# Kernel optimization log

Hardware: AMD Instinct MI355X
Metric: run time of the kernel (lower is better)

The kernel has to match this reference:

```python
import jax, jax.numpy as jnp
import numpy as np

N, E, F_NODE, F_EDGE, H = 50000, 800000, 64, 32, 64
NT, ET, ETE = 3, 4, 4  # num node types, num edge types, edge-type embedding dim
NEG = 0.2              # leaky_relu negative slope (PyG HEATConv default)


def hetero_lin(x, t, W, b):
    # per-type linear: x [N,in], t [N] int, W [T,in,out], b [T,out]
    outs = jnp.einsum('ni,tio->tno', x, W) + b[:, None, :]   # [T,N,out]
    return outs[t, jnp.arange(x.shape[0])]                   # [N,out]


def segment_softmax(logits, seg, num_segments):
    m = jax.ops.segment_max(logits, seg, num_segments=num_segments)
    ex = jnp.exp(logits - m[seg])
    s = jax.ops.segment_sum(ex, seg, num_segments=num_segments)
    return ex / (s[seg] + 1e-16)


def eheat_conv(x, src, dst, node_type, edge_type, edge_attr, Whl, bhl, Ete, Wea, Watt, Wlin):
    n = x.shape[0]
    h = hetero_lin(x, node_type, Whl, bhl)            # [N,H]
    ete = jax.nn.leaky_relu(Ete[edge_type], NEG)      # [E,ETE]
    ea = jax.nn.leaky_relu(edge_attr @ Wea, NEG)      # [E,H] edge embedding (returned)
    xi, xj = h[dst], h[src]                           # gather target/source node feats
    # attention logits = leaky_relu(att(cat([x_i, x_j, ete, ea]))); Watt split to avoid big concat
    Wi, Wj, Wt, We = Watt[:H], Watt[H:2 * H], Watt[2 * H:2 * H + ETE], Watt[2 * H + ETE:]
    logits = jax.nn.leaky_relu(xi @ Wi + xj @ Wj + ete @ Wt + ea @ We, NEG)[:, 0]  # [E]
    alpha = segment_softmax(logits, dst, n)           # softmax over incoming edges of dst
    # message = lin(cat([x_j, ea])) * alpha ; scatter-add at dst (heads=1, dropout eval=identity)
    msg = (xj @ Wlin[:H] + ea @ Wlin[H:]) * alpha[:, None]   # [E,H]
    out = jax.ops.segment_sum(msg, dst, num_segments=n)     # [N,H]
    return out, ea


def setup_inputs():
    key = jax.random.key(0)
    ks = jax.random.split(key, 40)
    def rnd(i, shape):
        return jax.random.normal(ks[i], shape, dtype=jnp.float32) * 0.1
    inp = {
        'x': jax.random.normal(ks[0], (N, F_NODE), dtype=jnp.float32),
        'edge_index': jax.random.randint(ks[1], (2, E), 0, N),
        'node_type': jax.random.randint(ks[2], (N,), 0, NT),
        'edge_type': jax.random.randint(ks[3], (E,), 0, ET),
        'edge_attr': jax.random.normal(ks[4], (E, F_EDGE), dtype=jnp.float32),
    }
    node_ins = [F_NODE, H, H]
    edge_ins = [F_EDGE, H, H]
    i = 5
    for l in range(3):
        inp[f'Whl{l+1}'] = rnd(i, (NT, node_ins[l], H)); i += 1
        inp[f'bhl{l+1}'] = jnp.zeros((NT, H), jnp.float32)
        inp[f'Ete{l+1}'] = rnd(i, (ET, ETE)); i += 1
        inp[f'Wea{l+1}'] = rnd(i, (edge_ins[l], H)); i += 1
        inp[f'Watt{l+1}'] = rnd(i, (2 * H + ETE + H, 1)); i += 1
        inp[f'Wlin{l+1}'] = rnd(i, (2 * H, H)); i += 1
    inp['Wnc'] = rnd(i, (NT, H, 1)); i += 1
    inp['bnc'] = jnp.zeros((NT, 1), jnp.float32)
    inp['Wec'] = rnd(i, (ET, H, 1)); i += 1
    inp['bec'] = jnp.zeros((ET, 1), jnp.float32)
    return inp


def reference(x, edge_index, node_type, edge_type, edge_attr,
              Whl1, bhl1, Ete1, Wea1, Watt1, Wlin1,
              Whl2, bhl2, Ete2, Wea2, Watt2, Wlin2,
              Whl3, bhl3, Ete3, Wea3, Watt3, Wlin3,
              Wnc, bnc, Wec, bec):
    src, dst = edge_index[0], edge_index[1]
    h, e = eheat_conv(x, src, dst, node_type, edge_type, edge_attr,
                      Whl1, bhl1, Ete1, Wea1, Watt1, Wlin1)
    h, e = jax.nn.relu(h), jax.nn.relu(e)   # dropout is identity in eval mode
    h, e = eheat_conv(h, src, dst, node_type, edge_type, e,
                      Whl2, bhl2, Ete2, Wea2, Watt2, Wlin2)
    h, e = jax.nn.relu(h), jax.nn.relu(e)
    h, e = eheat_conv(h, src, dst, node_type, edge_type, e,
                      Whl3, bhl3, Ete3, Wea3, Watt3, Wlin3)
    h, e = jax.nn.relu(h), jax.nn.relu(e)
    x_out = hetero_lin(h, node_type, Wnc, bnc)   # [N,1]
    e_out = hetero_lin(e, edge_type, Wec, bec)   # [E,1]
    return (x_out, e_out)
```

## Files before the change

### kernel.cpp

```cpp
#include <hip/hip_runtime.h>
#include <hip/hip_bf16.h>

#define NEG 0.2f
#define LRELU(x) ((x) > 0.f ? (x) : NEG*(x))

typedef __hip_bfloat16 bf16;
typedef __attribute__((ext_vector_type(8))) short short8v;
typedef __attribute__((ext_vector_type(4))) float f32x4;

__device__ __forceinline__ float b2f(bf16 v){ return __bfloat162float(v); }
__device__ __forceinline__ float ldf(const float* p, size_t i){ return p[i]; }
__device__ __forceinline__ float ldf(const bf16* p, size_t i){ return __bfloat162float(p[i]); }

__device__ __forceinline__ float wred(float v){
#pragma unroll
  for(int o=32;o>0;o>>=1) v += __shfl_down(v,o);
  return v;
}

__device__ __forceinline__ int atomAddI(int* p, int v){
  return __hip_atomic_fetch_add(p, v, __ATOMIC_RELAXED, __HIP_MEMORY_SCOPE_AGENT);
}


__global__ __launch_bounds__(256) void k_hist(
    const int* __restrict__ dst, int* __restrict__ deg, int nE)
{
  int e = blockIdx.x*blockDim.x + threadIdx.x;
  if (e >= nE) return;
  atomAddI(&deg[dst[e]], 1);
}

__global__ __launch_bounds__(1024) void k_scan(
    const int* __restrict__ deg, int* __restrict__ off, int nN)
{
  __shared__ int part[1024];
  int tid = threadIdx.x;
  int chunk = (nN + 1023) / 1024;
  int lo = tid*chunk, hi = min((tid+1)*chunk, nN);
  int s = 0;
  for (int i=lo;i<hi;i++) s += deg[i];
  part[tid] = s;
  __syncthreads();
  for (int d=1; d<1024; d<<=1){
    int v = (tid>=d) ? part[tid-d] : 0;
    __syncthreads();
    part[tid] += v;
    __syncthreads();
  }
  int run = (tid==0) ? 0 : part[tid-1];
  for (int i=lo;i<hi;i++){ off[i] = run; run += deg[i]; }
  if (tid==1023) off[nN] = part[1023];
}

__global__ __launch_bounds__(256) void k_scatter(
    const int* __restrict__ dst, const int* __restrict__ off,
    int* __restrict__ cnt, int* __restrict__ eid, int nE)
{
  int e = blockIdx.x*blockDim.x + threadIdx.x;
  if (e >= nE) return;
  int d = dst[e];
  int p = atomAddI(&cnt[d], 1);
  eid[off[d] + p] = e;
}

__global__ __launch_bounds__(256) void k_perm(
    const int* __restrict__ eid, const int* __restrict__ src,
    const int* __restrict__ dst, const int* __restrict__ ety,
    int* __restrict__ srcP, int* __restrict__ dstP, int* __restrict__ etyP, int nE)
{
  int i = blockIdx.x*blockDim.x + threadIdx.x;
  if (i >= nE) return;
  int e = eid[i];
  srcP[i] = src[e];
  dstP[i] = dst[e];
  etyP[i] = ety[e];
}


template<typename TIN, bool RELU_IN>
__global__ __launch_bounds__(256) void k_hlin(
    const TIN* __restrict__ xin, const int* __restrict__ ntype,
    const float* __restrict__ Whl, const float* __restrict__ bhl,
    const float* __restrict__ Watt,
    bf16* __restrict__ h, float* __restrict__ hi_s, float* __restrict__ hj_s,
    int nN)
{
  int wid  = (blockIdx.x*blockDim.x + threadIdx.x) >> 6;
  int lane = threadIdx.x & 63;
  if (wid >= nN) return;
  int t = ntype[wid];
  float xv = ldf(xin, (size_t)wid*64 + lane);
  if (RELU_IN) xv = fmaxf(xv, 0.f);
  const float* W = Whl + (size_t)t*4096;
  float acc = bhl[t*64 + lane];
#pragma unroll
  for (int i=0;i<64;i++) acc = fmaf(__shfl(xv, i), W[i*64 + lane], acc);
  h[(size_t)wid*64 + lane] = __float2bfloat16(acc);
  float pi = wred(acc * Watt[lane]);
  float pj = wred(acc * Watt[64 + lane]);
  if (lane==0){ hi_s[wid]=pi; hj_s[wid]=pj; }
}

__global__ __launch_bounds__(256) void k_bfrag(
    const float* __restrict__ W, bf16* __restrict__ frag, int KS)
{
  int t = blockIdx.x*blockDim.x + threadIdx.x;
  int total = 4*KS*64;
  if (t >= total) return;
  int lane = t & 63;
  int ks = (t>>6) % KS;
  int nt = (t>>6) / KS;
  int kb = lane>>4, col = lane&15;
#pragma unroll
  for (int j=0;j<8;j++){
    frag[((size_t)(nt*KS+ks)*64 + lane)*8 + j] =
      __float2bfloat16(W[(ks*32 + kb*8 + j)*64 + nt*16 + col]);
  }
}

template<int LAYER>
__global__ __launch_bounds__(256) void k_ea_mfma(
    const void* __restrict__ ain_, const int* __restrict__ eid,
    const bf16* __restrict__ bfrag, const float* __restrict__ Watt,
    const int* __restrict__ srcP, const int* __restrict__ dstP,
    const int* __restrict__ etyP, const float* __restrict__ Ete,
    const float* __restrict__ hi_s, const float* __restrict__ hj_s,
    bf16* __restrict__ eaS, float* __restrict__ exS,
    const float* __restrict__ Wec, const float* __restrict__ bec,
    float* __restrict__ e_out, int nE)
{
  constexpr int KS = (LAYER==0) ? 1 : 2;
  int wid  = (blockIdx.x*blockDim.x + threadIdx.x) >> 6;
  int lane = threadIdx.x & 63;
  int e0 = wid * 32;
  if (e0 >= nE) return;
  int row = lane & 15;
  int kb  = lane >> 4;

  short8v a[2][KS];
#pragma unroll
  for (int tl=0; tl<2; tl++){
    int er = min(e0 + tl*16 + row, nE-1);
    if (LAYER==0) {
      const float* A = (const float*)ain_;
      const float* p = A + (size_t)eid[er]*32 + kb*8;
#pragma unroll
      for (int j=0;j<8;j++){
        bf16 b = __float2bfloat16(p[j]);
        a[tl][0][j] = *reinterpret_cast<short*>(&b);
      }
    } else {
      const bf16* A = (const bf16*)ain_;
#pragma unroll
      for (int ks=0; ks<KS; ks++){
        short8v v = *reinterpret_cast<const short8v*>(
            reinterpret_cast<const short*>(A + (size_t)er*64 + ks*32 + kb*8));
#pragma unroll
        for (int j=0;j<8;j++) v[j] = (v[j] & (short)0x8000) ? (short)0 : v[j];
        a[tl][ks] = v;
      }
    }
  }

  f32x4 acc[2][4];
#pragma unroll
  for (int nt=0; nt<4; nt++){
    f32x4 c0 = {0.f,0.f,0.f,0.f}, c1 = {0.f,0.f,0.f,0.f};
#pragma unroll
    for (int ks=0; ks<KS; ks++){
      short8v b = *reinterpret_cast<const short8v*>(
          reinterpret_cast<const short*>(bfrag) + (((size_t)nt*KS + ks)*64 + lane)*8);
      c0 = __builtin_amdgcn_mfma_f32_16x16x32_bf16(a[0][ks], b, c0, 0, 0, 0);
      c1 = __builtin_amdgcn_mfma_f32_16x16x32_bf16(a[1][ks], b, c1, 0, 0, 0);
    }
#pragma unroll
    for (int r=0;r<4;r++){ c0[r] = LRELU(c0[r]); c1[r] = LRELU(c1[r]); }
    acc[0][nt] = c0; acc[1][nt] = c1;
  }

#pragma unroll
  for (int tl=0; tl<2; tl++){
#pragma unroll
    for (int r=0;r<4;r++){
      int e = e0 + tl*16 + kb*4 + r;
      if (e < nE){
#pragma unroll
        for (int nt=0;nt<4;nt++)
          eaS[(size_t)e*64 + nt*16 + row] = __float2bfloat16(acc[tl][nt][r]);
      }
    }
  }

#pragma unroll
  for (int tl=0; tl<2; tl++){
#pragma unroll
    for (int r=0;r<4;r++){
      int e = e0 + tl*16 + kb*4 + r;
      bool valid = (e < nE);
      int t = valid ? etyP[e] : 0;
      float lp = 0.f, pe = 0.f;
#pragma unroll
      for (int nt=0;nt<4;nt++) lp = fmaf(acc[tl][nt][r], Watt[132 + nt*16 + row], lp);
      if (LAYER==2){
#pragma unroll
        for (int nt=0;nt<4;nt++) pe = fmaf(fmaxf(acc[tl][nt][r],0.f), Wec[t*64 + nt*16 + row], pe);
      }
#pragma unroll
      for (int m=1;m<16;m<<=1){
        lp += __shfl_xor(lp, m);
        if (LAYER==2) pe += __shfl_xor(pe, m);
      }
      if (row == 0 && valid){
        int d = dstP[e], s = srcP[e];
        float wt = 0.f;
#pragma unroll
        for (int k=0;k<4;k++){ float v = Ete[t*4+k]; v = LRELU(v); wt = fmaf(v, Watt[128+k], wt); }
        float l = lp + hi_s[d] + hj_s[s] + wt;
        l = LRELU(l);
        exS[e] = __expf(fminf(l, 60.f));
        if (LAYER==2) e_out[eid[e]] = pe + bec[t];
      }
    }
  }
}

__global__ __launch_bounds__(256) void k_agg(
    const int* __restrict__ off, const int* __restrict__ srcP,
    const bf16* __restrict__ h, const bf16* __restrict__ eaS,
    const float* __restrict__ exS,
    bf16* __restrict__ uv, int nN)
{
  int wid  = (blockIdx.x*blockDim.x + threadIdx.x) >> 6;
  int lane = threadIdx.x & 63;
  if (wid >= nN) return;
  int beg = off[wid], end = off[wid+1];
  float au = 0.f, av = 0.f, ss = 0.f;
  int i = beg;
  for (; i+1 < end; i += 2){
    int   s0 = srcP[i],   s1 = srcP[i+1];
    float a0 = exS[i],    a1 = exS[i+1];
    float h0 = b2f(h[(size_t)s0*64 + lane]);
    float h1 = b2f(h[(size_t)s1*64 + lane]);
    float v0 = b2f(eaS[(size_t)i*64 + lane]);
    float v1 = b2f(eaS[(size_t)(i+1)*64 + lane]);
    au = fmaf(a0, h0, au); av = fmaf(a0, v0, av); ss += a0;
    au = fmaf(a1, h1, au); av = fmaf(a1, v1, av); ss += a1;
  }
  if (i < end){
    int s = srcP[i]; float a = exS[i];
    au = fmaf(a, b2f(h[(size_t)s*64 + lane]), au);
    av = fmaf(a, b2f(eaS[(size_t)i*64 + lane]), av);
    ss += a;
  }
  float inv = 1.f / (ss + 1e-16f);
  uv[(size_t)wid*128 + lane]      = __float2bfloat16(au * inv);
  uv[(size_t)wid*128 + 64 + lane] = __float2bfloat16(av * inv);
}

template<bool FINAL>
__global__ __launch_bounds__(256) void k_mm_mfma(
    const bf16* __restrict__ uv, const bf16* __restrict__ bfrag,
    float* __restrict__ out,
    const int* __restrict__ ntype, const float* __restrict__ Wnc,
    const float* __restrict__ bnc, float* __restrict__ xout, int nN)
{
  int wid  = (blockIdx.x*blockDim.x + threadIdx.x) >> 6;
  int lane = threadIdx.x & 63;
  int n0 = wid * 16;
  if (n0 >= nN) return;
  int row = lane & 15;
  int kb  = lane >> 4;
  int nr  = min(n0 + row, nN-1);

  short8v a[4];
#pragma unroll
  for (int ks=0; ks<4; ks++)
    a[ks] = *reinterpret_cast<const short8v*>(
        reinterpret_cast<const short*>(uv + (size_t)nr*128 + ks*32 + kb*8));

  f32x4 acc[4];
#pragma unroll
  for (int nt=0; nt<4; nt++){
    f32x4 c = {0.f,0.f,0.f,0.f};
#pragma unroll
    for (int ks=0; ks<4; ks++){
      short8v b = *reinterpret_cast<const short8v*>(
          reinterpret_cast<const short*>(bfrag) + (((size_t)nt*4 + ks)*64 + lane)*8);
      c = __builtin_amdgcn_mfma_f32_16x16x32_bf16(a[ks], b, c, 0, 0, 0);
    }
    acc[nt] = c;
  }

  if (!FINAL){
#pragma unroll
    for (int r=0;r<4;r++){
      int n = n0 + kb*4 + r;
      if (n < nN){
#pragma unroll
        for (int nt=0;nt<4;nt++)
          out[(size_t)n*64 + nt*16 + row] = acc[nt][r];
      }
    }
  } else {
#pragma unroll
    for (int r=0;r<4;r++){
      int n = n0 + kb*4 + r;
      bool valid = (n < nN);
      int t = valid ? ntype[n] : 0;
      float pe = 0.f;
#pragma unroll
      for (int nt=0;nt<4;nt++)
        pe = fmaf(fmaxf(acc[nt][r],0.f), Wnc[t*64 + nt*16 + row], pe);
#pragma unroll
      for (int m=1;m<16;m<<=1) pe += __shfl_xor(pe, m);
      if (row == 0 && valid) xout[n] = pe + bnc[t];
    }
  }
}

extern "C" void kernel_launch(void* const* d_in, const int* in_sizes, int n_in,
                              void* d_out, int out_size, void* d_ws, size_t ws_size,
                              hipStream_t stream) {
  const float* x      = (const float*)d_in[0];
  const int*   eidx   = (const int*) d_in[1];
  const int*   ntype  = (const int*) d_in[2];
  const int*   etype  = (const int*) d_in[3];
  const float* eattr  = (const float*)d_in[4];
  const float* Whl[3]  = {(const float*)d_in[5],  (const float*)d_in[11], (const float*)d_in[17]};
  const float* bhl[3]  = {(const float*)d_in[6],  (const float*)d_in[12], (const float*)d_in[18]};
  const float* Ete[3]  = {(const float*)d_in[7],  (const float*)d_in[13], (const float*)d_in[19]};
  const float* Wea[3]  = {(const float*)d_in[8],  (const float*)d_in[14], (const float*)d_in[20]};
  const float* Watt[3] = {(const float*)d_in[9],  (const float*)d_in[15], (const float*)d_in[21]};
  const float* Wlin[3] = {(const float*)d_in[10], (const float*)d_in[16], (const float*)d_in[22]};
  const float* Wnc = (const float*)d_in[23];
  const float* bnc = (const float*)d_in[24];
  const float* Wec = (const float*)d_in[25];
  const float* bec = (const float*)d_in[26];

  const int nN = in_sizes[2];
  const int nE = in_sizes[3];
  const int* srcI = eidx;
  const int* dstI = eidx + nE;

  float* ws = (float*)d_ws;
  size_t o = 0;
  bf16*  h      = (bf16*)(ws + o); o += (size_t)nN*32;
  float* outA   = ws + o;
  bf16*  uv     = (bf16*)(ws + o); o += (size_t)nN*64;
  float* hi_s   = ws + o;          o += (size_t)nN;
  float* hj_s   = ws + o;          o += (size_t)nN;
  float* exS    = ws + o;          o += (size_t)nE;
  bf16*  eaS    = (bf16*)(ws + o); o += (size_t)nE*32;
  int*   deg    = (int*)(ws + o);  o += (size_t)nN;
  int*   off    = (int*)(ws + o);  o += (size_t)nN + 1;
  int*   eid    = (int*)(ws + o);  o += (size_t)nE;
  int*   srcP   = (int*)(ws + o);  o += (size_t)nE;
  int*   dstP   = (int*)(ws + o);  o += (size_t)nE;
  int*   etyP   = (int*)(ws + o);  o += (size_t)nE;
  o = (o + 3) & ~(size_t)3;
  bf16*  bfrag  = (bf16*)(ws + o); o += (size_t)4096;

  dim3 blk(256);
  int nodeWB = (int)(((size_t)nN*64 + 255)/256);
  int edgeTB = (nE + 255)/256;
  int eaMB   = (int)(((size_t)((nE+31)/32)*64 + 255)/256);
  int mmMB   = (int)(((size_t)((nN+15)/16)*64 + 255)/256);

  hipMemsetAsync(deg, 0, (size_t)nN*4, stream);
  k_hist<<<edgeTB, blk, 0, stream>>>(dstI, deg, nE);
  k_scan<<<1, 1024, 0, stream>>>(deg, off, nN);
  hipMemsetAsync(deg, 0, (size_t)nN*4, stream);
  k_scatter<<<edgeTB, blk, 0, stream>>>(dstI, off, deg, eid, nE);
  k_perm<<<edgeTB, blk, 0, stream>>>(eid, srcI, dstI, etype, srcP, dstP, etyP, nE);

  float* xout = (float*)d_out;

  for (int L = 0; L < 3; ++L) {
    if (L == 0)
      k_hlin<float,false><<<nodeWB, blk, 0, stream>>>(x,    ntype, Whl[L], bhl[L], Watt[L], h, hi_s, hj_s, nN);
    else
      k_hlin<float,true ><<<nodeWB, blk, 0, stream>>>(outA, ntype, Whl[L], bhl[L], Watt[L], h, hi_s, hj_s, nN);

    int KS = (L==0) ? 1 : 2;
    k_bfrag<<<(4*KS*64 + 255)/256, blk, 0, stream>>>(Wea[L], bfrag, KS);
    if (L == 0)
      k_ea_mfma<0><<<eaMB, blk, 0, stream>>>(eattr, eid, bfrag, Watt[L], srcP, dstP, etyP, Ete[L],
                                             hi_s, hj_s, eaS, exS, nullptr, nullptr, nullptr, nE);
    else if (L == 1)
      k_ea_mfma<1><<<eaMB, blk, 0, stream>>>(eaS, eid, bfrag, Watt[L], srcP, dstP, etyP, Ete[L],
                                             hi_s, hj_s, eaS, exS, nullptr, nullptr, nullptr, nE);
    else
      k_ea_mfma<2><<<eaMB, blk, 0, stream>>>(eaS, eid, bfrag, Watt[L], srcP, dstP, etyP, Ete[L],
                                             hi_s, hj_s, eaS, exS, Wec, bec, xout + nN, nE);

    k_agg<<<nodeWB, blk, 0, stream>>>(off, srcP, h, eaS, exS, uv, nN);

    k_bfrag<<<(4*4*64 + 255)/256, blk, 0, stream>>>(Wlin[L], bfrag, 4);
    if (L < 2)
      k_mm_mfma<false><<<mmMB, blk, 0, stream>>>(uv, bfrag, outA, nullptr, nullptr, nullptr, nullptr, nN);
    else
      k_mm_mfma<true ><<<mmMB, blk, 0, stream>>>(uv, bfrag, nullptr, ntype, Wnc, bnc, xout, nN);
  }
}
```

Before: 913.1 us.

## Use MFMA for per-type node linear with nodes bucketed by type

Nodes are grouped by type into 32-padded buckets so the per-type hetero linear can run as bf16 MFMA tiles, with the attention projections folded into an extra output column tile. All weight fragments are precomputed once in a single prep kernel instead of per-layer k_bfrag launches. The attention logit combination is moved out of the edge MFMA kernel into a separate k_att kernel. This adds bucketing and prep kernels, one extra edge pass per layer, and bf16 rounding of the node inputs.

Measured after the change: 1.458 ms. 1.6x slower.

```diff
diff --git a/kernel.cpp b/kernel.cpp
--- a/kernel.cpp
+++ b/kernel.cpp
@@ -9,8 +9,6 @@
 typedef __attribute__((ext_vector_type(4))) float f32x4;
 
 __device__ __forceinline__ float b2f(bf16 v){ return __bfloat162float(v); }
-__device__ __forceinline__ float ldf(const float* p, size_t i){ return p[i]; }
-__device__ __forceinline__ float ldf(const bf16* p, size_t i){ return __bfloat162float(p[i]); }
 
 __device__ __forceinline__ float wred(float v){
 #pragma unroll
@@ -77,45 +75,146 @@
   etyP[i] = ety[e];
 }
 
-
-template<typename TIN, bool RELU_IN>
-__global__ __launch_bounds__(256) void k_hlin(
-    const TIN* __restrict__ xin, const int* __restrict__ ntype,
-    const float* __restrict__ Whl, const float* __restrict__ bhl,
-    const float* __restrict__ Watt,
-    bf16* __restrict__ h, float* __restrict__ hi_s, float* __restrict__ hj_s,
-    int nN)
+__global__ __launch_bounds__(256) void k_nhist(
+    const int* __restrict__ ntype, int* __restrict__ ndeg, int nN)
+{
+  int n = blockIdx.x*blockDim.x + threadIdx.x;
+  if (n >= nN) return;
+  atomAddI(&ndeg[ntype[n]], 1);
+}
+
+__global__ void k_npad(const int* __restrict__ ndeg, int* __restrict__ poffPad)
+{
+  if (threadIdx.x==0 && blockIdx.x==0){
+    int o = 0;
+#pragma unroll
+    for (int t=0;t<3;t++){ poffPad[t] = o; o += ((ndeg[t]+31)/32)*32; }
+    poffPad[3] = o;
+  }
+}
+
+__global__ __launch_bounds__(256) void k_nscatter(
+    const int* __restrict__ ntype, const int* __restrict__ poffPad,
+    int* __restrict__ ncnt, int* __restrict__ nPermPad, int nN)
+{
+  int n = blockIdx.x*blockDim.x + threadIdx.x;
+  if (n >= nN) return;
+  int t = ntype[n];
+  int p = atomAddI(&ncnt[t], 1);
+  nPermPad[poffPad[t] + p] = n;
+}
+
+struct BDesc { const float* W; const float* Wi; const float* Wj; int KS; int NT; int dstOff; };
+struct PrepArgs {
+  BDesc d[15];
+  const float* bhl[3];
+  const float* watt[3];
+};
+
+__global__ __launch_bounds__(256) void k_prep(
+    PrepArgs pa, bf16* __restrict__ fragBase, float* __restrict__ biasDot)
+{
+  int bid = blockIdx.x;
+  if (bid < 75){
+    int b = bid / 5;
+    int tid = (bid % 5)*256 + threadIdx.x;
+    BDesc d = pa.d[b];
+    int total = d.NT * d.KS * 64;
+    if (tid >= total) return;
+    int lane = tid & 63;
+    int ks = (tid>>6) % d.KS;
+    int nt = (tid>>6) / d.KS;
+    int kb = lane>>4, col16 = lane&15;
+    bf16* frag = fragBase + d.dstOff;
+#pragma unroll
+    for (int j=0;j<8;j++){
+      int k = ks*32 + kb*8 + j;
+      float val;
+      if (nt < 4) val = d.W[k*64 + nt*16 + col16];
+      else {
+        const float* v = (col16==0) ? d.Wi : (col16==1) ? d.Wj : nullptr;
+        val = 0.f;
+        if (v){ for (int c=0;c<64;c++) val = fmaf(d.W[k*64+c], v[c], val); }
+      }
+      frag[((size_t)(nt*d.KS+ks)*64 + lane)*8 + j] = __float2bfloat16(val);
+    }
+  } else {
+    int lane = threadIdx.x;
+    if (lane >= 64) return;
+    for (int idx=0; idx<18; idx++){
+      int L = idx/6, rem = idx%6, t = rem>>1, ij = rem&1;
+      float p = pa.bhl[L][t*64 + lane] * pa.watt[L][ij*64 + lane];
+      p = wred(p);
+      if (lane==0) biasDot[idx] = p;
+    }
+  }
+}
+
+
+template<bool RELU_IN>
+__global__ __launch_bounds__(256) void k_hlin_mfma(
+    const float* __restrict__ xin, const int* __restrict__ nPermPad,
+    const int* __restrict__ poffPad, const bf16* __restrict__ hlFragL,
+    const float* __restrict__ bhl, const float* __restrict__ biasDotL,
+    bf16* __restrict__ h, float* __restrict__ hi_s, float* __restrict__ hj_s)
 {
   int wid  = (blockIdx.x*blockDim.x + threadIdx.x) >> 6;
   int lane = threadIdx.x & 63;
-  if (wid >= nN) return;
-  int t = ntype[wid];
-  float xv = ldf(xin, (size_t)wid*64 + lane);
-  if (RELU_IN) xv = fmaxf(xv, 0.f);
-  const float* W = Whl + (size_t)t*4096;
-  float acc = bhl[t*64 + lane];
-#pragma unroll
-  for (int i=0;i<64;i++) acc = fmaf(__shfl(xv, i), W[i*64 + lane], acc);
-  h[(size_t)wid*64 + lane] = __float2bfloat16(acc);
-  float pi = wred(acc * Watt[lane]);
-  float pj = wred(acc * Watt[64 + lane]);
-  if (lane==0){ hi_s[wid]=pi; hj_s[wid]=pj; }
-}
-
-__global__ __launch_bounds__(256) void k_bfrag(
-    const float* __restrict__ W, bf16* __restrict__ frag, int KS)
-{
-  int t = blockIdx.x*blockDim.x + threadIdx.x;
-  int total = 4*KS*64;
-  if (t >= total) return;
-  int lane = t & 63;
-  int ks = (t>>6) % KS;
-  int nt = (t>>6) / KS;
-  int kb = lane>>4, col = lane&15;
-#pragma unroll
-  for (int j=0;j<8;j++){
-    frag[((size_t)(nt*KS+ks)*64 + lane)*8 + j] =
-      __float2bfloat16(W[(ks*32 + kb*8 + j)*64 + nt*16 + col]);
+  int n0 = wid * 32;
+  if (n0 >= poffPad[3]) return;
+  int t = (n0 >= poffPad[1]) + (n0 >= poffPad[2]);
+  const bf16* frag = hlFragL + (size_t)t*5120;
+  int row = lane & 15, kb = lane >> 4;
+
+  short8v a[2][2];
+#pragma unroll
+  for (int tl=0; tl<2; tl++){
+    int orig = nPermPad[n0 + tl*16 + row];
+    const float* p = xin + (size_t)max(orig,0)*64;
+#pragma unroll
+    for (int ks=0; ks<2; ks++){
+#pragma unroll
+      for (int j=0;j<8;j++){
+        float v = p[ks*32 + kb*8 + j];
+        if (RELU_IN) v = fmaxf(v, 0.f);
+        bf16 b = __float2bfloat16(v);
+        a[tl][ks][j] = *reinterpret_cast<short*>(&b);
+      }
+    }
+  }
+
+  f32x4 acc[2][5];
+#pragma unroll
+  for (int nt=0; nt<5; nt++){
+    f32x4 c0 = {0.f,0.f,0.f,0.f}, c1 = {0.f,0.f,0.f,0.f};
+#pragma unroll
+    for (int ks=0; ks<2; ks++){
+      short8v b = *reinterpret_cast<const short8v*>(
+          reinterpret_cast<const short*>(frag) + (((size_t)nt*2 + ks)*64 + lane)*8);
+      c0 = __builtin_amdgcn_mfma_f32_16x16x32_bf16(a[0][ks], b, c0, 0, 0, 0);
+      c1 = __builtin_amdgcn_mfma_f32_16x16x32_bf16(a[1][ks], b, c1, 0, 0, 0);
+    }
+    acc[0][nt] = c0; acc[1][nt] = c1;
+  }
+
+  float bb[4];
+#pragma unroll
+  for (int nt=0;nt<4;nt++) bb[nt] = bhl[t*64 + nt*16 + row];
+  float bdi = biasDotL[t*2+0], bdj = biasDotL[t*2+1];
+
+#pragma unroll
+  for (int tl=0; tl<2; tl++){
+#pragma unroll
+    for (int r=0;r<4;r++){
+      int orig = nPermPad[n0 + tl*16 + kb*4 + r];
+      if (orig >= 0){
+#pragma unroll
+        for (int nt=0;nt<4;nt++)
+          h[(size_t)orig*64 + nt*16 + row] = __float2bfloat16(acc[tl][nt][r] + bb[nt]);
+        if (row==0) hi_s[orig] = acc[tl][4][r] + bdi;
+        if (row==1) hj_s[orig] = acc[tl][4][r] + bdj;
+      }
+    }
   }
 }
 
@@ -123,10 +222,8 @@
 __global__ __launch_bounds__(256) void k_ea_mfma(
     const void* __restrict__ ain_, const int* __restrict__ eid,
     const bf16* __restrict__ bfrag, const float* __restrict__ Watt,
-    const int* __restrict__ srcP, const int* __restrict__ dstP,
-    const int* __restrict__ etyP, const float* __restrict__ Ete,
-    const float* __restrict__ hi_s, const float* __restrict__ hj_s,
-    bf16* __restrict__ eaS, float* __restrict__ exS,
+    const int* __restrict__ etyP,
+    bf16* __restrict__ eaS, float* __restrict__ lp,
     const float* __restrict__ Wec, const float* __restrict__ bec,
     float* __restrict__ e_out, int nE)
 {
@@ -198,31 +295,43 @@
     for (int r=0;r<4;r++){
       int e = e0 + tl*16 + kb*4 + r;
       bool valid = (e < nE);
-      int t = valid ? etyP[e] : 0;
-      float lp = 0.f, pe = 0.f;
-#pragma unroll
-      for (int nt=0;nt<4;nt++) lp = fmaf(acc[tl][nt][r], Watt[132 + nt*16 + row], lp);
-      if (LAYER==2){
-#pragma unroll
-        for (int nt=0;nt<4;nt++) pe = fmaf(fmaxf(acc[tl][nt][r],0.f), Wec[t*64 + nt*16 + row], pe);
+      float lpv = 0.f, pe = 0.f;
+      int t = 0;
+      if (LAYER==2) t = valid ? etyP[e] : 0;
+#pragma unroll
+      for (int nt=0;nt<4;nt++){
+        lpv = fmaf(acc[tl][nt][r], Watt[132 + nt*16 + row], lpv);
+        if (LAYER==2) pe = fmaf(fmaxf(acc[tl][nt][r],0.f), Wec[t*64 + nt*16 + row], pe);
       }
 #pragma unroll
       for (int m=1;m<16;m<<=1){
-        lp += __shfl_xor(lp, m);
+        lpv += __shfl_xor(lpv, m);
         if (LAYER==2) pe += __shfl_xor(pe, m);
       }
       if (row == 0 && valid){
-        int d = dstP[e], s = srcP[e];
-        float wt = 0.f;
-#pragma unroll
-        for (int k=0;k<4;k++){ float v = Ete[t*4+k]; v = LRELU(v); wt = fmaf(v, Watt[128+k], wt); }
-        float l = lp + hi_s[d] + hj_s[s] + wt;
-        l = LRELU(l);
-        exS[e] = __expf(fminf(l, 60.f));
+        lp[e] = lpv;
         if (LAYER==2) e_out[eid[e]] = pe + bec[t];
       }
     }
   }
+}
+
+__global__ __launch_bounds__(256) void k_att(
+    const int* __restrict__ srcP, const int* __restrict__ dstP,
+    const int* __restrict__ etyP, const float* __restrict__ Ete,
+    const float* __restrict__ Watt,
+    const float* __restrict__ hi_s, const float* __restrict__ hj_s,
+    float* __restrict__ lpex, int nE)
+{
+  int e = blockIdx.x*blockDim.x + threadIdx.x;
+  if (e >= nE) return;
+  int d = dstP[e], s = srcP[e], t = etyP[e];
+  float wt = 0.f;
+#pragma unroll
+  for (int k=0;k<4;k++){ float v = Ete[t*4+k]; v = LRELU(v); wt = fmaf(v, Watt[128+k], wt); }
+  float l = lpex[e] + hi_s[d] + hj_s[s] + wt;
+  l = LRELU(l);
+  lpex[e] = __expf(fminf(l, 60.f));
 }
 
 __global__ __launch_bounds__(256) void k_agg(
@@ -350,7 +459,7 @@
   bf16*  uv     = (bf16*)(ws + o); o += (size_t)nN*64;
   float* hi_s   = ws + o;          o += (size_t)nN;
   float* hj_s   = ws + o;          o += (size_t)nN;
-  float* exS    = ws + o;          o += (size_t)nE;
+  float* lpex   = ws + o;          o += (size_t)nE;
   bf16*  eaS    = (bf16*)(ws + o); o += (size_t)nE*32;
   int*   deg    = (int*)(ws + o);  o += (size_t)nN;
   int*   off    = (int*)(ws + o);  o += (size_t)nN + 1;
@@ -358,13 +467,24 @@
   int*   srcP   = (int*)(ws + o);  o += (size_t)nE;
   int*   dstP   = (int*)(ws + o);  o += (size_t)nE;
   int*   etyP   = (int*)(ws + o);  o += (size_t)nE;
+  int*   ndeg   = (int*)(ws + o);  o += 4;
+  int*   ncnt   = (int*)(ws + o);  o += 4;
+  int*   poffPad= (int*)(ws + o);  o += 4;
+  int*   nPermPad=(int*)(ws + o);  o += (size_t)nN + 96;
   o = (o + 3) & ~(size_t)3;
-  bf16*  bfrag  = (bf16*)(ws + o); o += (size_t)4096;
+  bf16*  fragB  = (bf16*)(ws + o); o += 40448;
+  float* biasDot= ws + o;          o += 18;
+
+  const int eaOff[3] = {0, 2048, 6144};
+  const int hlOff = 10240;
+  const int wlOff = 56320;
 
   dim3 blk(256);
   int nodeWB = (int)(((size_t)nN*64 + 255)/256);
   int edgeTB = (nE + 255)/256;
+  int nodeTB = (nN + 255)/256;
   int eaMB   = (int)(((size_t)((nE+31)/32)*64 + 255)/256);
+  int hlMB   = (int)(((size_t)((nN+96+31)/32)*64 + 255)/256);
   int mmMB   = (int)(((size_t)((nN+15)/16)*64 + 255)/256);
 
   hipMemsetAsync(deg, 0, (size_t)nN*4, stream);
@@ -374,32 +494,53 @@
   k_scatter<<<edgeTB, blk, 0, stream>>>(dstI, off, deg, eid, nE);
   k_perm<<<edgeTB, blk, 0, stream>>>(eid, srcI, dstI, etype, srcP, dstP, etyP, nE);
 
+  hipMemsetAsync(ndeg, 0, 8*4, stream);
+  k_nhist<<<nodeTB, blk, 0, stream>>>(ntype, ndeg, nN);
+  k_npad<<<1, 64, 0, stream>>>(ndeg, poffPad);
+  hipMemsetAsync(nPermPad, 0xFF, ((size_t)nN+96)*4, stream);
+  k_nscatter<<<nodeTB, blk, 0, stream>>>(ntype, poffPad, ncnt, nPermPad, nN);
+
+  PrepArgs pa;
+  pa.d[0] = {Wea[0], nullptr, nullptr, 1, 4, eaOff[0]};
+  pa.d[1] = {Wea[1], nullptr, nullptr, 2, 4, eaOff[1]};
+  pa.d[2] = {Wea[2], nullptr, nullptr, 2, 4, eaOff[2]};
+  for (int L=0; L<3; L++)
+    for (int t=0; t<3; t++)
+      pa.d[3 + L*3 + t] = {Whl[L] + (size_t)t*4096, Watt[L], Watt[L]+64, 2, 5, hlOff + (L*3+t)*5120};
+  for (int L=0; L<3; L++)
+    pa.d[12 + L] = {Wlin[L], nullptr, nullptr, 4, 4, wlOff + L*8192};
+  for (int L=0; L<3; L++){ pa.bhl[L] = bhl[L]; pa.watt[L] = Watt[L]; }
+  k_prep<<<76, blk, 0, stream>>>(pa, fragB, biasDot);
+
   float* xout = (float*)d_out;
 
   for (int L = 0; L < 3; ++L) {
     if (L == 0)
-      k_hlin<float,false><<<nodeWB, blk, 0, stream>>>(x,    ntype, Whl[L], bhl[L], Watt[L], h, hi_s, hj_s, nN);
+      k_hlin_mfma<false><<<hlMB, blk, 0, stream>>>(x,    nPermPad, poffPad, fragB + hlOff + L*3*5120,
+                                                   bhl[L], biasDot + L*6, h, hi_s, hj_s);
     else
-      k_hlin<float,true ><<<nodeWB, blk, 0, stream>>>(outA, ntype, Whl[L], bhl[L], Watt[L], h, hi_s, hj_s, nN);
-
-    int KS = (L==0) ? 1 : 2;
-    k_bfrag<<<(4*KS*64 + 255)/256, blk, 0, stream>>>(Wea[L], bfrag, KS);
+      k_hlin_mfma<true ><<<hlMB, blk, 0, stream>>>(outA, nPermPad, poffPad, fragB + hlOff + L*3*5120,
+                                                   bhl[L], biasDot + L*6, h, hi_s, hj_s);
+
     if (L == 0)
-      k_ea_mfma<0><<<eaMB, blk, 0, stream>>>(eattr, eid, bfrag, Watt[L], srcP, dstP, etyP, Ete[L],
-                                             hi_s, hj_s, eaS, exS, nullptr, nullptr, nullptr, nE);
+      k_ea_mfma<0><<<eaMB, blk, 0, stream>>>(eattr, eid, fragB + eaOff[L], Watt[L], etyP,
+                                             eaS, lpex, nullptr, nullptr, nullptr, nE);
     else if (L == 1)
-      k_ea_mfma<1><<<eaMB, blk, 0, stream>>>(eaS, eid, bfrag, Watt[L], srcP, dstP, etyP, Ete[L],
-                                             hi_s, hj_s, eaS, exS, nullptr, nullptr, nullptr, nE);
+      k_ea_mfma<1><<<eaMB, blk, 0, stream>>>(eaS, eid, fragB + eaOff[L], Watt[L], etyP,
+                                             eaS, lpex, nullptr, nullptr, nullptr, nE);
     else
-      k_ea_mfma<2><<<eaMB, blk, 0, stream>>>(eaS, eid, bfrag, Watt[L], srcP, dstP, etyP, Ete[L],
-                                             hi_s, hj_s, eaS, exS, Wec, bec, xout + nN, nE);
-
-    k_agg<<<nodeWB, blk, 0, stream>>>(off, srcP, h, eaS, exS, uv, nN);
-
-    k_bfrag<<<(4*4*64 + 255)/256, blk, 0, stream>>>(Wlin[L], bfrag, 4);
+      k_ea_mfma<2><<<eaMB, blk, 0, stream>>>(eaS, eid, fragB + eaOff[L], Watt[L], etyP,
+                                             eaS, lpex, Wec, bec, xout + nN, nE);
+
+    k_att<<<edgeTB, blk, 0, stream>>>(srcP, dstP, etyP, Ete[L], Watt[L], hi_s, hj_s, lpex, nE);
+
+    k_agg<<<nodeWB, blk, 0, stream>>>(off, srcP, h, eaS, lpex, uv, nN);
+
     if (L < 2)
-      k_mm_mfma<false><<<mmMB, blk, 0, stream>>>(uv, bfrag, outA, nullptr, nullptr, nullptr, nullptr, nN);
+      k_mm_mfma<false><<<mmMB, blk, 0, stream>>>(uv, fragB + wlOff + L*8192, outA,
+                                                 nullptr, nullptr, nullptr, nullptr, nN);
     else
-      k_mm_mfma<true ><<<mmMB, blk, 0, stream>>>(uv, bfrag, nullptr, ntype, Wnc, bnc, xout, nN);
-  }
-}
+      k_mm_mfma<true ><<<mmMB, blk, 0, stream>>>(uv, fragB + wlOff + L*8192, nullptr,
+                                                 ntype, Wnc, bnc, xout, nN);
+  }
+}
```
